# Kernel tuning notes

Hardware: AMD Instinct MI355X
Metric: run time of the kernel (lower is better)

The kernel has to match this reference:

```python
import jax, jax.numpy as jnp
import numpy as np

VOCAB, D_MODEL, HIDDEN, NUM_CLASSES = 32000, 512, 768, 2
B, S = 64, 512


def _gru_dir(x_sbd, Wi, Wh, bi, bh, reverse):
    # x_sbd: [S,B,D]; Wi: [3H,D]; Wh: [3H,H]; bi,bh: [3H]
    H = Wh.shape[1]
    xg = jnp.einsum('sbd,gd->sbg', x_sbd, Wi) + bi  # [S,B,3H] precomputed input gates

    def step(h, xg_t):
        hg = h @ Wh.T + bh
        xr, xz, xn = jnp.split(xg_t, 3, axis=-1)
        hr, hz, hn = jnp.split(hg, 3, axis=-1)
        r = jax.nn.sigmoid(xr + hr)
        z = jax.nn.sigmoid(xz + hz)
        n = jnp.tanh(xn + r * hn)
        h_new = (1.0 - z) * n + z * h
        return h_new, None

    h0 = jnp.zeros((x_sbd.shape[1], H), dtype=x_sbd.dtype)
    h_last, _ = jax.lax.scan(step, h0, xg, reverse=reverse)
    return h_last  # [B,H]


def setup_inputs() -> dict:
    key = jax.random.key(0)
    ks = jax.random.split(key, 16)
    sd, sh = 1.0 / np.sqrt(D_MODEL), 1.0 / np.sqrt(HIDDEN)
    inp = {
        'input_ids': jax.random.randint(ks[0], (B, S), 0, VOCAB),
        'emb': jax.random.normal(ks[1], (VOCAB, D_MODEL), jnp.float32),
        'Wi_f': jax.random.uniform(ks[2], (3 * HIDDEN, D_MODEL), jnp.float32, -sd, sd),
        'Wh_f': jax.random.uniform(ks[3], (3 * HIDDEN, HIDDEN), jnp.float32, -sh, sh),
        'bi_f': jax.random.uniform(ks[4], (3 * HIDDEN,), jnp.float32, -sh, sh),
        'bh_f': jax.random.uniform(ks[5], (3 * HIDDEN,), jnp.float32, -sh, sh),
        'Wi_b': jax.random.uniform(ks[6], (3 * HIDDEN, D_MODEL), jnp.float32, -sd, sd),
        'Wh_b': jax.random.uniform(ks[7], (3 * HIDDEN, HIDDEN), jnp.float32, -sh, sh),
        'bi_b': jax.random.uniform(ks[8], (3 * HIDDEN,), jnp.float32, -sh, sh),
        'bh_b': jax.random.uniform(ks[9], (3 * HIDDEN,), jnp.float32, -sh, sh),
        'W1': jax.random.uniform(ks[10], (HIDDEN, 2 * HIDDEN), jnp.float32, -sh, sh),
        'b1': jnp.zeros((HIDDEN,), jnp.float32),
        'W2': jax.random.uniform(ks[11], (NUM_CLASSES, HIDDEN), jnp.float32, -sh, sh),
        'b2': jnp.zeros((NUM_CLASSES,), jnp.float32),
    }
    return inp


def reference(input_ids, emb, Wi_f, Wh_f, bi_f, bh_f, Wi_b, Wh_b, bi_b, bh_b, W1, b1, W2, b2):
    x = emb[input_ids]                      # [B,S,D]
    x_sbd = jnp.transpose(x, (1, 0, 2))     # [S,B,D]
    h_fwd = _gru_dir(x_sbd, Wi_f, Wh_f, bi_f, bh_f, reverse=False)
    h_bwd = _gru_dir(x_sbd, Wi_b, Wh_b, bi_b, bh_b, reverse=True)
    h = jnp.concatenate([h_fwd, h_bwd], axis=-1)  # [B,2H]
    hid = jax.nn.relu(h @ W1.T + b1)
    logits = hid @ W2.T + b2                # [B,num_classes]
    return logits
```

## Files before the change

### kernel.cpp

```cpp
#include <hip/hip_runtime.h>
#include <hip/hip_bf16.h>
#include <cstdint>

typedef _Float16 h2 __attribute__((ext_vector_type(2)));
typedef _Float16 h4 __attribute__((ext_vector_type(4)));
typedef _Float16 h8 __attribute__((ext_vector_type(8)));
typedef float f4 __attribute__((ext_vector_type(4)));
typedef unsigned int u32x4 __attribute__((ext_vector_type(4)));
typedef unsigned long long u64;

#define S_LEN 512
#define BATCH 64
#define DM    512
#define HID   768

union h4u { u64 u; h4 v; };

static __device__ __forceinline__ h8 pack8(float4 a, float4 b) {
  h8 v;
  v[0] = (_Float16)a.x; v[1] = (_Float16)a.y;
  v[2] = (_Float16)a.z; v[3] = (_Float16)a.w;
  v[4] = (_Float16)b.x; v[5] = (_Float16)b.y;
  v[6] = (_Float16)b.z; v[7] = (_Float16)b.w;
  return v;
}

static __device__ __forceinline__ h8 ldfrag(const _Float16* S, int row, int ke) {
  int byte = (row << 7) + (ke << 1);
  byte ^= (row & 7) << 4;
  return *(const h8*)((const char*)S + byte);
}
static __device__ __forceinline__ void stfrag(_Float16* S, int row, int ke, h8 v) {
  int byte = (row << 7) + (ke << 1);
  byte ^= (row & 7) << 4;
  *(h8*)((char*)S + byte) = v;
}

__global__ __launch_bounds__(256) void gemm1_kernel(
    const int* __restrict__ ids, const float* __restrict__ emb,
    const float* __restrict__ Wi_f, const float* __restrict__ bi_f,
    const float* __restrict__ Wi_b, const float* __restrict__ bi_b,
    int s0_f, int s0_b,
    _Float16* __restrict__ xg_f, _Float16* __restrict__ xg_b)
{
  const int mt  = blockIdx.x;
  const int nt  = blockIdx.y;
  const int dir = blockIdx.z;
  const float* __restrict__ Wi = dir ? Wi_b : Wi_f;
  const float* __restrict__ bi = dir ? bi_b : bi_f;
  _Float16*   __restrict__ xg  = dir ? xg_b : xg_f;
  const int s0 = dir ? s0_b : s0_f;

  __shared__ _Float16 Ws[128 * 64];
  __shared__ _Float16 Es[128 * 64];
  __shared__ int ids_s[128];

  const int tid = threadIdx.x;
  if (tid < 128) {
    ids_s[tid] = ids[(tid & 63) * S_LEN + s0 + mt * 2 + (tid >> 6)];
  }

  const int w  = tid >> 6;
  const int L  = tid & 63;
  const int lh = L >> 4;
  const int ln = L & 15;
  const int wn = (w >> 1) * 64;
  const int wm = (w & 1) * 64;

  const int r  = tid >> 1;
  const int kh = (tid & 1) * 32;

  f4 acc[4][4];
#pragma unroll
  for (int i = 0; i < 4; ++i)
#pragma unroll
    for (int j = 0; j < 4; ++j) { acc[i][j][0]=0.f; acc[i][j][1]=0.f; acc[i][j][2]=0.f; acc[i][j][3]=0.f; }

  __syncthreads();

  for (int kt = 0; kt < DM; kt += 64) {
    {
      const float* srcW = Wi + (size_t)(nt * 128 + r) * DM + kt + kh;
      const float* srcE = emb + (size_t)ids_s[r] * DM + kt + kh;
      float4 w0 = ((const float4*)srcW)[0], w1 = ((const float4*)srcW)[1];
      float4 w2 = ((const float4*)srcW)[2], w3 = ((const float4*)srcW)[3];
      float4 w4 = ((const float4*)srcW)[4], w5 = ((const float4*)srcW)[5];
      float4 w6 = ((const float4*)srcW)[6], w7 = ((const float4*)srcW)[7];
      float4 e0 = ((const float4*)srcE)[0], e1 = ((const float4*)srcE)[1];
      float4 e2 = ((const float4*)srcE)[2], e3 = ((const float4*)srcE)[3];
      float4 e4 = ((const float4*)srcE)[4], e5 = ((const float4*)srcE)[5];
      float4 e6 = ((const float4*)srcE)[6], e7 = ((const float4*)srcE)[7];
      stfrag(Ws, r, kh + 0,  pack8(w0, w1));
      stfrag(Ws, r, kh + 8,  pack8(w2, w3));
      stfrag(Ws, r, kh + 16, pack8(w4, w5));
      stfrag(Ws, r, kh + 24, pack8(w6, w7));
      stfrag(Es, r, kh + 0,  pack8(e0, e1));
      stfrag(Es, r, kh + 8,  pack8(e2, e3));
      stfrag(Es, r, kh + 16, pack8(e4, e5));
      stfrag(Es, r, kh + 24, pack8(e6, e7));
    }
    __syncthreads();
#pragma unroll
    for (int ks = 0; ks < 2; ++ks) {
      h8 af[4], bf[4];
#pragma unroll
      for (int i = 0; i < 4; ++i) af[i] = ldfrag(Ws, wn + i * 16 + ln, ks * 32 + lh * 8);
#pragma unroll
      for (int j = 0; j < 4; ++j) bf[j] = ldfrag(Es, wm + j * 16 + ln, ks * 32 + lh * 8);
#pragma unroll
      for (int i = 0; i < 4; ++i)
#pragma unroll
        for (int j = 0; j < 4; ++j)
          acc[i][j] = __builtin_amdgcn_mfma_f32_16x16x32_f16(af[i], bf[j], acc[i][j], 0, 0, 0);
    }
    __syncthreads();
  }

#pragma unroll
  for (int i = 0; i < 4; ++i) {
    const int n_g = nt * 128 + wn + i * 16 + lh * 4;
    const int gate = n_g / 768;
    const int jj = n_g - gate * 768;
    const f4 bv = *(const f4*)&bi[n_g];
#pragma unroll
    for (int j = 0; j < 4; ++j) {
      const int m = mt * 128 + wm + j * 16 + ln;
      const int sl = m >> 6, b = m & 63;
      h4 v;
#pragma unroll
      for (int rr = 0; rr < 4; ++rr) v[rr] = (_Float16)(acc[i][j][rr] + bv[rr]);
      *(h4*)&xg[(((size_t)sl * 3 + gate) * 64 + b) * 768 + jj] = v;
    }
  }
}

__global__ __launch_bounds__(256, 1) void scan_mfma_kernel(
    const float* __restrict__ Wh_f, const float* __restrict__ bh_f,
    const float* __restrict__ Wh_b, const float* __restrict__ bh_b,
    const _Float16* __restrict__ xg_f, const _Float16* __restrict__ xg_b,
    char* __restrict__ hx,
    unsigned* __restrict__ tags,
    float* __restrict__ hfin,
    int step0, int nsteps)
{
  const int blk = blockIdx.x;
  const int dir = blk / 48;
  const int l   = blk - dir * 48;
  const int bg  = l / 12;
  const int jb  = l - bg * 12;

  const float* __restrict__ Wh = dir ? Wh_b : Wh_f;
  const float* __restrict__ bh = dir ? bh_b : bh_f;
  const _Float16* __restrict__ xg = dir ? xg_b : xg_f;
  char*     payB = hx + (size_t)dir * 2 * 64 * 96 * 16;
  unsigned* tagB = tags + dir * 64 * 16;
  float*    hfd  = hfin + (size_t)dir * 64 * 768;

  const int tid = threadIdx.x;
  const int w   = tid >> 6;
  const int L   = tid & 63;
  const int lh  = L >> 4;
  const int ln  = L & 15;
  const int jt  = jb * 4 + w;
  const int jrow = jt * 16 + ln;
  const int j0l  = jt * 16 + lh * 4;
  const int bglob = bg * 16 + ln;
  const int bb  = tid >> 4;
  const int qi  = tid & 15;

  __shared__ __align__(16) unsigned char hs[96 * 256];

  h8 A[3][24];
#pragma unroll
  for (int g = 0; g < 3; ++g)
#pragma unroll
    for (int ks = 0; ks < 24; ++ks) {
      const float* src = Wh + (size_t)(g * 768 + jrow) * 768 + ks * 32 + lh * 8;
      float4 w0 = ((const float4*)src)[0];
      float4 w1 = ((const float4*)src)[1];
      A[g][ks] = pack8(w0, w1);
    }

  f4 bhv[3];
#pragma unroll
  for (int g = 0; g < 3; ++g) bhv[g] = *(const f4*)&bh[g * 768 + j0l];

  f4 hm;
  if (step0 == 0) { hm[0]=0.f; hm[1]=0.f; hm[2]=0.f; hm[3]=0.f; }
  else {
    const float* src = &hfd[(size_t)bglob * 768 + j0l];
    asm volatile("global_load_dwordx4 %0, %1, off sc0 sc1\n\t"
                 "s_waitcnt vmcnt(0)"
                 : "=&v"(hm) : "v"(src) : "memory");
  }

  unsigned* mytag = tagB + (bg * 16 + bb) * 16;
  const char* pcb = payB;
  const size_t pslot = ((size_t)bglob * 96 + jt * 2 + (lh >> 1)) * 16
                     + (size_t)(lh & 1) * 8;
  const int swb = (bb ^ (qi & 7)) * 16;

  for (int t = 0; t < nsteps; ++t) {
    const int sg = step0 + t;
    const int pin = sg & 1, pout = pin ^ 1;

    const int lsl = dir ? (nsteps - 1 - t) : t;
    const _Float16* xrow = xg + (((size_t)lsl * 3) * 64 + bglob) * 768 + j0l;
    h4 xr4 = *(const h4*)xrow;
    h4 xz4 = *(const h4*)(xrow + (size_t)64 * 768);
    h4 xn4 = *(const h4*)(xrow + (size_t)2 * 64 * 768);

    {
      u32x4 t0, t1, t2;
      for (;;) {
        asm volatile(
          "global_load_dwordx4 %0, %3, off sc0 sc1\n\t"
          "global_load_dwordx4 %1, %4, off sc0 sc1\n\t"
          "global_load_dwordx4 %2, %5, off sc0 sc1\n\t"
          "s_waitcnt vmcnt(0)"
          : "=&v"(t0), "=&v"(t1), "=&v"(t2)
          : "v"(mytag), "v"(mytag + 4), "v"(mytag + 8)
          : "memory");
        unsigned m01 = min(min(t0[0], t0[1]), min(t0[2], t0[3]));
        unsigned m23 = min(min(t1[0], t1[1]), min(t1[2], t1[3]));
        unsigned m45 = min(min(t2[0], t2[1]), min(t2[2], t2[3]));
        if (min(min(m01, m23), m45) >= (unsigned)sg) break;
      }
    }

    u32x4 p0, p1, p2, p3, p4, p5;
    {
      const char* pc = pcb + (((size_t)pin * 64 + bg * 16 + bb) * 96 + qi) * 16;
      asm volatile(
        "global_load_dwordx4 %0, %6, off sc0 sc1\n\t"
        "global_load_dwordx4 %1, %7, off sc0 sc1\n\t"
        "global_load_dwordx4 %2, %8, off sc0 sc1\n\t"
        "global_load_dwordx4 %3, %9, off sc0 sc1\n\t"
        "global_load_dwordx4 %4, %10, off sc0 sc1\n\t"
        "global_load_dwordx4 %5, %11, off sc0 sc1\n\t"
        "s_waitcnt vmcnt(0)"
        : "=&v"(p0), "=&v"(p1), "=&v"(p2), "=&v"(p3), "=&v"(p4), "=&v"(p5)
        : "v"(pc), "v"(pc + 16*16), "v"(pc + 32*16), "v"(pc + 48*16),
          "v"(pc + 64*16), "v"(pc + 80*16)
        : "memory");
    }

    *(u32x4*)(hs + (qi +  0) * 256 + swb) = p0;
    *(u32x4*)(hs + (qi + 16) * 256 + swb) = p1;
    *(u32x4*)(hs + (qi + 32) * 256 + swb) = p2;
    *(u32x4*)(hs + (qi + 48) * 256 + swb) = p3;
    *(u32x4*)(hs + (qi + 64) * 256 + swb) = p4;
    *(u32x4*)(hs + (qi + 80) * 256 + swb) = p5;
    __syncthreads();

    f4 Cr, Cz, Cn;
    Cr[0]=0.f;Cr[1]=0.f;Cr[2]=0.f;Cr[3]=0.f;
    Cz = Cr; Cn = Cr;
#pragma unroll
    for (int ks = 0; ks < 24; ++ks) {
      const int g = ks * 4 + lh;
      h8 Bf = *(const h8*)(hs + g * 256 + ((ln ^ (g & 7)) * 16));
      Cr = __builtin_amdgcn_mfma_f32_16x16x32_f16(A[0][ks], Bf, Cr, 0, 0, 0);
      Cz = __builtin_amdgcn_mfma_f32_16x16x32_f16(A[1][ks], Bf, Cz, 0, 0, 0);
      Cn = __builtin_amdgcn_mfma_f32_16x16x32_f16(A[2][ks], Bf, Cn, 0, 0, 0);
    }

    f4 hnew;
    h4u st;
#pragma unroll
    for (int r = 0; r < 4; ++r) {
      float rr = 1.f / (1.f + __expf(-((float)xr4[r] + Cr[r] + bhv[0][r])));
      float zz = 1.f / (1.f + __expf(-((float)xz4[r] + Cz[r] + bhv[1][r])));
      float nn = tanhf((float)xn4[r] + rr * (Cn[r] + bhv[2][r]));
      hnew[r] = (1.f - zz) * nn + zz * hm[r];
      st.v[r] = (_Float16)hnew[r];
    }
    hm = hnew;

    {
      char* dst = payB + (size_t)pout * 64 * 96 * 16 + pslot;
      asm volatile("global_store_dwordx2 %0, %1, off sc0 sc1"
                   :: "v"(dst), "v"(st.u) : "memory");
      asm volatile("s_waitcnt vmcnt(0)" ::: "memory");
    }
    __syncthreads();
    if (tid < 16) {
      unsigned tv = (unsigned)(sg + 1);
      unsigned* ta = tagB + (bg * 16 + tid) * 16 + jb;
      asm volatile("global_store_dword %0, %1, off sc0 sc1"
                   :: "v"(ta), "v"(tv) : "memory");
    }
  }

  {
    float* dst = &hfd[(size_t)bglob * 768 + j0l];
    asm volatile("global_store_dwordx4 %0, %1, off sc0 sc1"
                 :: "v"(dst), "v"(hm) : "memory");
  }
}

__global__ __launch_bounds__(256) void mlp1_kernel(
    const float* __restrict__ hfin, const float* __restrict__ W1,
    const float* __restrict__ b1, float* __restrict__ hid)
{
  const int c = blockIdx.x * 4 + (threadIdx.x >> 6);
  const int b = threadIdx.x & 63;
  const float* __restrict__ hf = hfin + (size_t)b * 768;
  const float* __restrict__ hb = hfin + (size_t)(64 + b) * 768;
  const float* __restrict__ w = W1 + (size_t)c * 1536;
  float acc = b1[c];
  for (int k = 0; k < 768; k += 4) {
    float4 hv = *(const float4*)&hf[k];
    float4 wv = *(const float4*)&w[k];
    acc += hv.x * wv.x + hv.y * wv.y + hv.z * wv.z + hv.w * wv.w;
  }
  for (int k = 0; k < 768; k += 4) {
    float4 hv = *(const float4*)&hb[k];
    float4 wv = *(const float4*)&w[768 + k];
    acc += hv.x * wv.x + hv.y * wv.y + hv.z * wv.z + hv.w * wv.w;
  }
  hid[(size_t)c * 64 + b] = fmaxf(acc, 0.f);
}

__global__ void mlp2_kernel(const float* __restrict__ hid,
                            const float* __restrict__ W2,
                            const float* __restrict__ b2,
                            float* __restrict__ out)
{
  const int tid = threadIdx.x;
  const int b = tid & 63, cls = tid >> 6;
  const float* __restrict__ w = W2 + cls * 768;
  float acc = b2[cls];
  for (int k = 0; k < 768; ++k) acc += hid[(size_t)k * 64 + b] * w[k];
  out[b * 2 + cls] = acc;
}

extern "C" void kernel_launch(void* const* d_in, const int* in_sizes, int n_in,
                              void* d_out, int out_size, void* d_ws, size_t ws_size,
                              hipStream_t stream)
{
  const int*   ids  = (const int*)d_in[0];
  const float* emb  = (const float*)d_in[1];
  const float* Wi_f = (const float*)d_in[2];
  const float* Wh_f = (const float*)d_in[3];
  const float* bi_f = (const float*)d_in[4];
  const float* bh_f = (const float*)d_in[5];
  const float* Wi_b = (const float*)d_in[6];
  const float* Wh_b = (const float*)d_in[7];
  const float* bi_b = (const float*)d_in[8];
  const float* bh_b = (const float*)d_in[9];
  const float* W1   = (const float*)d_in[10];
  const float* b1   = (const float*)d_in[11];
  const float* W2   = (const float*)d_in[12];
  const float* b2   = (const float*)d_in[13];
  float* out = (float*)d_out;

  const size_t B_HX   = (size_t)2 * 2 * 64 * 96 * 16;
  const size_t B_TAG  = (size_t)2 * 64 * 16 * 4;
  const size_t B_HFIN = (size_t)2 * 64 * 768 * 4;
  const size_t B_HID  = (size_t)HID * BATCH * 4;
  const size_t state_bytes = B_HX + B_TAG + B_HFIN + B_HID;

  int CH = 512;
  while (CH > 8) {
    size_t need = (size_t)4 * CH * 64 * 2304 + state_bytes;
    if (need <= ws_size) break;
    CH >>= 1;
  }
  const size_t SZ_XG = (size_t)CH * 64 * 2304;

  char* ws = (char*)d_ws;
  _Float16* xg_f = (_Float16*)ws;
  _Float16* xg_b = xg_f + SZ_XG;
  char*     hx   = (char*)(xg_b + SZ_XG);
  unsigned* tags = (unsigned*)(hx + B_HX);
  float*    hfin = (float*)((char*)tags + B_TAG);
  float*    hid  = (float*)((char*)hfin + B_HFIN);

  (void)hipMemsetAsync(hx, 0, state_bytes, stream);

  const int nch = 512 / CH;
  for (int c = 0; c < nch; ++c) {
    const int s0f = c * CH;
    const int s0b = 512 - (c + 1) * CH;
    gemm1_kernel<<<dim3(CH / 2, 18, 2), 256, 0, stream>>>(
        ids, emb, Wi_f, bi_f, Wi_b, bi_b, s0f, s0b, xg_f, xg_b);
    scan_mfma_kernel<<<96, 256, 0, stream>>>(
        Wh_f, bh_f, Wh_b, bh_b, xg_f, xg_b, hx, tags, hfin, c * CH, CH);
  }
  mlp1_kernel<<<192, 256, 0, stream>>>(hfin, W1, b1, hid);
  mlp2_kernel<<<1, 128, 0, stream>>>(hid, W2, b2, out);
}
```

Baseline: 2.677 ms.

## Embed step tags in fp16 hidden-state payload bits to drop separate flag round-trip

The scan kernel previously published each step's fp16 hidden state and then, after a wait and a block barrier, wrote separate per-block tag words that consumers polled before loading the payload. Now the hidden state is clamped to [-1,1] so bit 14 of every fp16 is always zero. A 4-bit step counter is encoded into those bits, and consumers spin directly on the payload until all embedded bits match the expected step, then mask them off. This removes one global memory round-trip and a store-wait per step in the latency-bound recurrence. The cost is heavier spin loads and reliance on per-8-byte store atomicity and value-range assumptions. Values near ±1 lose nothing, since the clamp is a no-op for the actual GRU output range.

```diff
diff --git a/kernel.cpp b/kernel.cpp
--- a/kernel.cpp
+++ b/kernel.cpp
@@ -6,8 +6,8 @@
 typedef _Float16 h4 __attribute__((ext_vector_type(4)));
 typedef _Float16 h8 __attribute__((ext_vector_type(8)));
 typedef float f4 __attribute__((ext_vector_type(4)));
-typedef unsigned int u32x4 __attribute__((ext_vector_type(4)));
 typedef unsigned long long u64;
+typedef unsigned int u32;
 
 #define S_LEN 512
 #define BATCH 64
@@ -139,7 +139,6 @@
     const float* __restrict__ Wh_b, const float* __restrict__ bh_b,
     const _Float16* __restrict__ xg_f, const _Float16* __restrict__ xg_b,
     char* __restrict__ hx,
-    unsigned* __restrict__ tags,
     float* __restrict__ hfin,
     int step0, int nsteps)
 {
@@ -152,9 +151,8 @@
   const float* __restrict__ Wh = dir ? Wh_b : Wh_f;
   const float* __restrict__ bh = dir ? bh_b : bh_f;
   const _Float16* __restrict__ xg = dir ? xg_b : xg_f;
-  char*     payB = hx + (size_t)dir * 2 * 64 * 96 * 16;
-  unsigned* tagB = tags + dir * 64 * 16;
-  float*    hfd  = hfin + (size_t)dir * 64 * 768;
+  char*  payB = hx + (size_t)dir * 2 * 64 * 1536;
+  float* hfd  = hfin + (size_t)dir * 64 * 768;
 
   const int tid = threadIdx.x;
   const int w   = tid >> 6;
@@ -194,10 +192,8 @@
                  : "=&v"(hm) : "v"(src) : "memory");
   }
 
-  unsigned* mytag = tagB + (bg * 16 + bb) * 16;
-  const char* pcb = payB;
-  const size_t pslot = ((size_t)bglob * 96 + jt * 2 + (lh >> 1)) * 16
-                     + (size_t)(lh & 1) * 8;
+  char* const pslot = payB + (size_t)bglob * 1536 + (size_t)(jt * 4 + lh) * 8;
+  const char* const crow = payB + (size_t)(bg * 16 + bb) * 1536 + qi * 16;
   const int swb = (bb ^ (qi & 7)) * 16;
 
   for (int t = 0; t < nsteps; ++t) {
@@ -210,47 +206,50 @@
     h4 xz4 = *(const h4*)(xrow + (size_t)64 * 768);
     h4 xn4 = *(const h4*)(xrow + (size_t)2 * 64 * 768);
 
+    const u32 texp = (u32)sg & 15u;
+    const u32 e0 = ((texp & 1u) << 14) | ((texp & 2u) << 29);
+    const u32 e1 = ((texp & 4u) << 12) | ((texp & 8u) << 27);
+    const char* pc = crow + (size_t)pin * 64 * 1536;
+    u64 q0,q1,q2,q3,q4,q5,q6,q7,q8,q9,q10,q11;
+    for (;;) {
+      asm volatile(
+        "global_load_dwordx2 %0, %12, off sc0 sc1\n\t"
+        "global_load_dwordx2 %1, %12, off offset:8 sc0 sc1\n\t"
+        "global_load_dwordx2 %2, %13, off sc0 sc1\n\t"
+        "global_load_dwordx2 %3, %13, off offset:8 sc0 sc1\n\t"
+        "global_load_dwordx2 %4, %14, off sc0 sc1\n\t"
+        "global_load_dwordx2 %5, %14, off offset:8 sc0 sc1\n\t"
+        "global_load_dwordx2 %6, %15, off sc0 sc1\n\t"
+        "global_load_dwordx2 %7, %15, off offset:8 sc0 sc1\n\t"
+        "global_load_dwordx2 %8, %16, off sc0 sc1\n\t"
+        "global_load_dwordx2 %9, %16, off offset:8 sc0 sc1\n\t"
+        "global_load_dwordx2 %10, %17, off sc0 sc1\n\t"
+        "global_load_dwordx2 %11, %17, off offset:8 sc0 sc1\n\t"
+        "s_waitcnt vmcnt(0)"
+        : "=&v"(q0), "=&v"(q1), "=&v"(q2), "=&v"(q3), "=&v"(q4), "=&v"(q5),
+          "=&v"(q6), "=&v"(q7), "=&v"(q8), "=&v"(q9), "=&v"(q10), "=&v"(q11)
+        : "v"(pc), "v"(pc + 256), "v"(pc + 512),
+          "v"(pc + 768), "v"(pc + 1024), "v"(pc + 1280)
+        : "memory");
+      u32 bad = 0;
+      u64 qs[12] = {q0,q1,q2,q3,q4,q5,q6,q7,q8,q9,q10,q11};
+#pragma unroll
+      for (int i = 0; i < 12; ++i) {
+        u32 lo = (u32)qs[i], hi = (u32)(qs[i] >> 32);
+        bad |= ((lo & 0x40004000u) ^ e0) | ((hi & 0x40004000u) ^ e1);
+      }
+      if (bad == 0) break;
+    }
     {
-      u32x4 t0, t1, t2;
-      for (;;) {
-        asm volatile(
-          "global_load_dwordx4 %0, %3, off sc0 sc1\n\t"
-          "global_load_dwordx4 %1, %4, off sc0 sc1\n\t"
-          "global_load_dwordx4 %2, %5, off sc0 sc1\n\t"
-          "s_waitcnt vmcnt(0)"
-          : "=&v"(t0), "=&v"(t1), "=&v"(t2)
-          : "v"(mytag), "v"(mytag + 4), "v"(mytag + 8)
-          : "memory");
-        unsigned m01 = min(min(t0[0], t0[1]), min(t0[2], t0[3]));
-        unsigned m23 = min(min(t1[0], t1[1]), min(t1[2], t1[3]));
-        unsigned m45 = min(min(t2[0], t2[1]), min(t2[2], t2[3]));
-        if (min(min(m01, m23), m45) >= (unsigned)sg) break;
+      const u64 CM = 0xBFFFBFFFBFFFBFFFull;
+      u64 qa[12] = {q0&CM,q1&CM,q2&CM,q3&CM,q4&CM,q5&CM,q6&CM,q7&CM,q8&CM,q9&CM,q10&CM,q11&CM};
+#pragma unroll
+      for (int i = 0; i < 6; ++i) {
+        u64* d = (u64*)(hs + (qi + 16 * i) * 256 + swb);
+        d[0] = qa[2 * i];
+        d[1] = qa[2 * i + 1];
       }
     }
-
-    u32x4 p0, p1, p2, p3, p4, p5;
-    {
-      const char* pc = pcb + (((size_t)pin * 64 + bg * 16 + bb) * 96 + qi) * 16;
-      asm volatile(
-        "global_load_dwordx4 %0, %6, off sc0 sc1\n\t"
-        "global_load_dwordx4 %1, %7, off sc0 sc1\n\t"
-        "global_load_dwordx4 %2, %8, off sc0 sc1\n\t"
-        "global_load_dwordx4 %3, %9, off sc0 sc1\n\t"
-        "global_load_dwordx4 %4, %10, off sc0 sc1\n\t"
-        "global_load_dwordx4 %5, %11, off sc0 sc1\n\t"
-        "s_waitcnt vmcnt(0)"
-        : "=&v"(p0), "=&v"(p1), "=&v"(p2), "=&v"(p3), "=&v"(p4), "=&v"(p5)
-        : "v"(pc), "v"(pc + 16*16), "v"(pc + 32*16), "v"(pc + 48*16),
-          "v"(pc + 64*16), "v"(pc + 80*16)
-        : "memory");
-    }
-
-    *(u32x4*)(hs + (qi +  0) * 256 + swb) = p0;
-    *(u32x4*)(hs + (qi + 16) * 256 + swb) = p1;
-    *(u32x4*)(hs + (qi + 32) * 256 + swb) = p2;
-    *(u32x4*)(hs + (qi + 48) * 256 + swb) = p3;
-    *(u32x4*)(hs + (qi + 64) * 256 + swb) = p4;
-    *(u32x4*)(hs + (qi + 80) * 256 + swb) = p5;
     __syncthreads();
 
     f4 Cr, Cz, Cn;
@@ -258,8 +257,8 @@
     Cz = Cr; Cn = Cr;
 #pragma unroll
     for (int ks = 0; ks < 24; ++ks) {
-      const int g = ks * 4 + lh;
-      h8 Bf = *(const h8*)(hs + g * 256 + ((ln ^ (g & 7)) * 16));
+      const int p = ks * 4 + lh;
+      h8 Bf = *(const h8*)(hs + p * 256 + ((ln ^ (p & 7)) * 16));
       Cr = __builtin_amdgcn_mfma_f32_16x16x32_f16(A[0][ks], Bf, Cr, 0, 0, 0);
       Cz = __builtin_amdgcn_mfma_f32_16x16x32_f16(A[1][ks], Bf, Cz, 0, 0, 0);
       Cn = __builtin_amdgcn_mfma_f32_16x16x32_f16(A[2][ks], Bf, Cn, 0, 0, 0);
@@ -273,23 +272,21 @@
       float zz = 1.f / (1.f + __expf(-((float)xz4[r] + Cz[r] + bhv[1][r])));
       float nn = tanhf((float)xn4[r] + rr * (Cn[r] + bhv[2][r]));
       hnew[r] = (1.f - zz) * nn + zz * hm[r];
-      st.v[r] = (_Float16)hnew[r];
+      st.v[r] = (_Float16)fminf(1.f, fmaxf(-1.f, hnew[r]));
     }
     hm = hnew;
 
     {
-      char* dst = payB + (size_t)pout * 64 * 96 * 16 + pslot;
+      const u32 tw = (u32)(sg + 1) & 15u;
+      u32 lo = (u32)st.u, hi = (u32)(st.u >> 32);
+      lo |= ((tw & 1u) << 14) | ((tw & 2u) << 29);
+      hi |= ((tw & 4u) << 12) | ((tw & 8u) << 27);
+      u64 pv = ((u64)hi << 32) | lo;
+      char* dst = pslot + (size_t)pout * 64 * 1536;
       asm volatile("global_store_dwordx2 %0, %1, off sc0 sc1"
-                   :: "v"(dst), "v"(st.u) : "memory");
-      asm volatile("s_waitcnt vmcnt(0)" ::: "memory");
+                   :: "v"(dst), "v"(pv) : "memory");
     }
     __syncthreads();
-    if (tid < 16) {
-      unsigned tv = (unsigned)(sg + 1);
-      unsigned* ta = tagB + (bg * 16 + tid) * 16 + jb;
-      asm volatile("global_store_dword %0, %1, off sc0 sc1"
-                   :: "v"(ta), "v"(tv) : "memory");
-    }
   }
 
   {
@@ -355,11 +352,10 @@
   const float* b2   = (const float*)d_in[13];
   float* out = (float*)d_out;
 
-  const size_t B_HX   = (size_t)2 * 2 * 64 * 96 * 16;
-  const size_t B_TAG  = (size_t)2 * 64 * 16 * 4;
+  const size_t B_HX   = (size_t)2 * 2 * 64 * 1536;
   const size_t B_HFIN = (size_t)2 * 64 * 768 * 4;
   const size_t B_HID  = (size_t)HID * BATCH * 4;
-  const size_t state_bytes = B_HX + B_TAG + B_HFIN + B_HID;
+  const size_t state_bytes = B_HX + B_HFIN + B_HID;
 
   int CH = 512;
   while (CH > 8) {
@@ -373,8 +369,7 @@
   _Float16* xg_f = (_Float16*)ws;
   _Float16* xg_b = xg_f + SZ_XG;
   char*     hx   = (char*)(xg_b + SZ_XG);
-  unsigned* tags = (unsigned*)(hx + B_HX);
-  float*    hfin = (float*)((char*)tags + B_TAG);
+  float*    hfin = (float*)(hx + B_HX);
   float*    hid  = (float*)((char*)hfin + B_HFIN);
 
   (void)hipMemsetAsync(hx, 0, state_bytes, stream);
@@ -386,7 +381,7 @@
     gemm1_kernel<<<dim3(CH / 2, 18, 2), 256, 0, stream>>>(
         ids, emb, Wi_f, bi_f, Wi_b, bi_b, s0f, s0b, xg_f, xg_b);
     scan_mfma_kernel<<<96, 256, 0, stream>>>(
-        Wh_f, bh_f, Wh_b, bh_b, xg_f, xg_b, hx, tags, hfin, c * CH, CH);
+        Wh_f, bh_f, Wh_b, bh_b, xg_f, xg_b, hx, hfin, c * CH, CH);
   }
   mlp1_kernel<<<192, 256, 0, stream>>>(hfin, W1, b1, hid);
   mlp2_kernel<<<1, 128, 0, stream>>>(hid, W2, b2, out);
```

Result: faster. 2.593 ms (-3.1%).
